# Kernel optimization log

Hardware: AMD Instinct MI355X
Metric: run time of the kernel (lower is better)

The kernel has to match this reference:

```python
import jax, jax.numpy as jnp
import numpy as np

N, E, HID, H_SA, H_MHA, L = 20000, 320000, 128, 4, 4, 32
MLP_HID = 4 * HID
EPS = 1e-6


def _ln(x, eps=EPS):
    mu = jnp.mean(x, axis=-1, keepdims=True)
    var = jnp.var(x, axis=-1, keepdims=True)
    return (x - mu) * jax.lax.rsqrt(var + eps)


def _modulate(x, shift, scale):
    return x * (1.0 + scale) + shift


def setup_inputs() -> dict:
    key = jax.random.key(0)
    ks = jax.random.split(key, 32)
    s = 0.02
    inp = {
        'x': jax.random.normal(ks[0], (N, HID), jnp.float32),
        'edge_index': jax.random.randint(ks[1], (2, E), 0, N, jnp.int64),
        't': jax.random.normal(ks[2], (N, HID), jnp.float32),
        'text_emb': jax.random.normal(ks[3], (N, L, HID), jnp.float32),
        # TransformerConv (per-head out_channels = HID, concat=False)
        'sa_q_w': jax.random.normal(ks[4], (HID, H_SA * HID), jnp.float32) * s,
        'sa_q_b': jnp.zeros((H_SA * HID,), jnp.float32),
        'sa_k_w': jax.random.normal(ks[5], (HID, H_SA * HID), jnp.float32) * s,
        'sa_k_b': jnp.zeros((H_SA * HID,), jnp.float32),
        'sa_v_w': jax.random.normal(ks[6], (HID, H_SA * HID), jnp.float32) * s,
        'sa_v_b': jnp.zeros((H_SA * HID,), jnp.float32),
        'sa_skip_w': jax.random.normal(ks[7], (HID, HID), jnp.float32) * s,
        'sa_skip_b': jnp.zeros((HID,), jnp.float32),
        # norm3 affine
        'n3_g': jnp.ones((HID,), jnp.float32),
        'n3_b': jnp.zeros((HID,), jnp.float32),
        # MultiheadAttention
        'mha_q_w': jax.random.normal(ks[8], (HID, HID), jnp.float32) * s,
        'mha_q_b': jnp.zeros((HID,), jnp.float32),
        'mha_k_w': jax.random.normal(ks[9], (HID, HID), jnp.float32) * s,
        'mha_k_b': jnp.zeros((HID,), jnp.float32),
        'mha_v_w': jax.random.normal(ks[10], (HID, HID), jnp.float32) * s,
        'mha_v_b': jnp.zeros((HID,), jnp.float32),
        'mha_o_w': jax.random.normal(ks[11], (HID, HID), jnp.float32) * s,
        'mha_o_b': jnp.zeros((HID,), jnp.float32),
        # MLP
        'fc1_w': jax.random.normal(ks[12], (HID, MLP_HID), jnp.float32) * s,
        'fc1_b': jnp.zeros((MLP_HID,), jnp.float32),
        'fc2_w': jax.random.normal(ks[13], (MLP_HID, HID), jnp.float32) * s,
        'fc2_b': jnp.zeros((HID,), jnp.float32),
        # adaLN modulation
        'ada_w': jax.random.normal(ks[14], (HID, 6 * HID), jnp.float32) * s,
        'ada_b': jnp.zeros((6 * HID,), jnp.float32),
    }
    return inp


def reference(x, edge_index, t, text_emb,
              sa_q_w, sa_q_b, sa_k_w, sa_k_b, sa_v_w, sa_v_b, sa_skip_w, sa_skip_b,
              n3_g, n3_b,
              mha_q_w, mha_q_b, mha_k_w, mha_k_b, mha_v_w, mha_v_b, mha_o_w, mha_o_b,
              fc1_w, fc1_b, fc2_w, fc2_b, ada_w, ada_b):
    n = x.shape[0]
    # adaLN: SiLU -> Linear -> chunk(6)
    mod = jax.nn.silu(t) @ ada_w + ada_b  # [N, 6*HID]
    shift_msa, scale_msa, gate_msa, shift_mlp, scale_mlp, gate_mlp = jnp.split(mod, 6, axis=1)

    # ---- graph self-attention (PyG TransformerConv, concat=False) ----
    xm = _modulate(_ln(x), shift_msa, scale_msa)  # [N, HID]
    q = (xm @ sa_q_w + sa_q_b).reshape(n, H_SA, HID)
    k = (xm @ sa_k_w + sa_k_b).reshape(n, H_SA, HID)
    v = (xm @ sa_v_w + sa_v_b).reshape(n, H_SA, HID)
    src, dst = edge_index[0], edge_index[1]  # messages flow src -> dst
    # per-edge attention logits [E, H]
    logits = jnp.einsum('ehd,ehd->eh', q[dst], k[src]) / jnp.sqrt(jnp.float32(HID))
    m = jax.ops.segment_max(logits, dst, num_segments=n)          # [N, H]
    ex = jnp.exp(logits - m[dst])                                  # [E, H]
    den = jax.ops.segment_sum(ex, dst, num_segments=n)            # [N, H]
    alpha = ex / den[dst]                                          # [E, H]
    agg = jax.ops.segment_sum(alpha[:, :, None] * v[src], dst, num_segments=n)  # [N, H, HID]
    sa_out = agg.mean(axis=1) + (xm @ sa_skip_w + sa_skip_b)       # concat=False -> head mean, + root skip
    x = x + gate_msa * sa_out

    # ---- cross attention: each node attends over its text memory ----
    qn = _ln(x) * n3_g + n3_b                                      # norm3 (affine)
    dh = HID // H_MHA
    qh = (qn @ mha_q_w + mha_q_b).reshape(n, H_MHA, dh)
    kh = (text_emb @ mha_k_w + mha_k_b).reshape(n, L, H_MHA, dh)
    vh = (text_emb @ mha_v_w + mha_v_b).reshape(n, L, H_MHA, dh)
    scores = jnp.einsum('nhd,nlhd->nhl', qh, kh) / jnp.sqrt(jnp.float32(dh))
    attn = jax.nn.softmax(scores, axis=-1)
    ctx = jnp.einsum('nhl,nlhd->nhd', attn, vh).reshape(n, HID)
    x = x + (ctx @ mha_o_w + mha_o_b)

    # ---- gated MLP ----
    xm2 = _modulate(_ln(x), shift_mlp, scale_mlp)
    h = jax.nn.gelu(xm2 @ fc1_w + fc1_b, approximate=True)
    x = x + gate_mlp * (h @ fc2_w + fc2_b)
    return x
```

## Files before the change

### kernel.cpp

```cpp
#include <hip/hip_runtime.h>
#include <hip/hip_bf16.h>
#include <math.h>

using ushort8 = __attribute__((ext_vector_type(8))) unsigned short;
using short8  = __attribute__((ext_vector_type(8))) short;
using f32x4   = __attribute__((ext_vector_type(4))) float;
using f32x2   = __attribute__((ext_vector_type(2))) float;

__device__ __forceinline__ float bf2f(unsigned short u) {
    union { unsigned int i; float f; } c; c.i = ((unsigned int)u) << 16; return c.f;
}
__device__ __forceinline__ unsigned short f2bf(float f) {
    __hip_bfloat16 h = __float2bfloat16(f);
    return *reinterpret_cast<unsigned short*>(&h);
}
__device__ __forceinline__ float silu_f(float x) { return x / (1.f + __expf(-x)); }
__device__ __forceinline__ float gelu_f(float x) {
    float x3 = x * x * x;
    return 0.5f * x * (1.f + tanhf(0.7978845608028654f * (x + 0.044715f * x3)));
}

constexpr int QKV_STRIDE_B = 2304;

template<int WM, int AIN, int PRE, int EPI, int OUTBF>
__global__ __launch_bounds__(256) void gemm_mfma(
    const void* __restrict__ Ain, const unsigned short* __restrict__ Wt,
    const float* __restrict__ bias, void* __restrict__ Cout,
    const float* __restrict__ res, const void* __restrict__ gatep,
    int Nrows, int K, int M)
{
    constexpr int BM = 32 * WM;
    __shared__ unsigned short As[BM][64];
    __shared__ unsigned short Bs[128][64];
    const int tid = threadIdx.x;
    const int row0 = blockIdx.x * BM;
    const int col0 = blockIdx.y * 128;
    const int lane = tid & 63;
    const int wid  = tid >> 6;
    const int wr = (wid >> 1) * 16 * WM;
    const int wc = (wid & 1) * 64;
    const int lr = lane & 15;
    const int lk = lane >> 4;

    f32x4 acc[WM][4];
#pragma unroll
    for (int i = 0; i < WM; i++)
#pragma unroll
        for (int j = 0; j < 4; j++) acc[i][j] = (f32x4)0.f;

    for (int k0 = 0; k0 < K; k0 += 64) {
#pragma unroll
        for (int i = 0; i < BM * 8 / 256; i++) {
            int f = tid + i * 256;
            int m = f >> 3, b = f & 7;
            int r = row0 + m;
            ushort8 h;
            if (r < Nrows) {
                if (AIN == 1) {
                    h = *(const ushort8*)((const unsigned short*)Ain + (size_t)r * K + k0 + b * 8);
                } else {
                    const float* ap = (const float*)Ain + (size_t)r * K + k0 + b * 8;
                    float4 p0 = *(const float4*)ap;
                    float4 p1 = *(const float4*)(ap + 4);
                    float v[8] = {p0.x, p0.y, p0.z, p0.w, p1.x, p1.y, p1.z, p1.w};
                    if (PRE == 1) {
#pragma unroll
                        for (int j = 0; j < 8; j++) v[j] = silu_f(v[j]);
                    }
#pragma unroll
                    for (int j = 0; j < 8; j++) h[j] = f2bf(v[j]);
                }
            } else {
#pragma unroll
                for (int j = 0; j < 8; j++) h[j] = 0;
            }
            *(ushort8*)&As[m][((b ^ (m & 7))) * 8] = h;
        }
#pragma unroll
        for (int i = 0; i < 4; i++) {
            int f = tid + i * 256;
            int n = f >> 3, b = f & 7;
            ushort8 w = *(const ushort8*)(Wt + (size_t)(col0 + n) * K + k0 + b * 8);
            *(ushort8*)&Bs[n][((b ^ (n & 7))) * 8] = w;
        }
        __syncthreads();

        short8 afr[WM][2], bfr[4][2];
#pragma unroll
        for (int fr = 0; fr < WM; fr++)
#pragma unroll
            for (int s = 0; s < 2; s++) {
                int m = wr + fr * 16 + lr;
                int blk = (s * 4 + lk) ^ (m & 7);
                afr[fr][s] = *(const short8*)&As[m][blk * 8];
            }
#pragma unroll
        for (int fc = 0; fc < 4; fc++)
#pragma unroll
            for (int s = 0; s < 2; s++) {
                int n = wc + fc * 16 + lr;
                int blk = (s * 4 + lk) ^ (n & 7);
                bfr[fc][s] = *(const short8*)&Bs[n][blk * 8];
            }
#pragma unroll
        for (int fr = 0; fr < WM; fr++)
#pragma unroll
            for (int fc = 0; fc < 4; fc++)
#pragma unroll
                for (int s = 0; s < 2; s++)
                    acc[fr][fc] = __builtin_amdgcn_mfma_f32_16x16x32_bf16(
                        afr[fr][s], bfr[fc][s], acc[fr][fc], 0, 0, 0);
        __syncthreads();
    }

#pragma unroll
    for (int fr = 0; fr < WM; fr++) {
#pragma unroll
        for (int fc = 0; fc < 4; fc++) {
#pragma unroll
            for (int r = 0; r < 4; r++) {
                int row = row0 + wr + fr * 16 + (lane >> 4) * 4 + r;
                if (row >= Nrows) continue;
                int col = col0 + wc + fc * 16 + (lane & 15);
                float val = acc[fr][fc][r] + bias[col];
                if (EPI == 4) {
                    unsigned char* rowp = (unsigned char*)Cout + (size_t)row * QKV_STRIDE_B;
                    if (col < 512) {
                        *(unsigned short*)(rowp + 2 * col) = f2bf(val);
                    } else if (col < 1536) {
                        int p = __builtin_amdgcn_cvt_pk_fp8_f32(val, 0.f, 0, false);
                        rowp[1024 + (col - 512)] = (unsigned char)(p & 0xff);
                    } else {
                        *(unsigned short*)(rowp + 2048 + 2 * (col - 1536)) = f2bf(val);
                    }
                } else {
                    size_t idx = (size_t)row * M + col;
                    if (EPI == 1) val = gelu_f(val);
                    else if (EPI == 2) val = res[idx] + val;
                    else if (EPI == 3) val = res[idx] +
                        bf2f(((const unsigned short*)gatep)[(size_t)row * 768 + col]) * val;
                    if (OUTBF) ((unsigned short*)Cout)[idx] = f2bf(val);
                    else       ((float*)Cout)[idx] = val;
                }
            }
        }
    }
}

__global__ __launch_bounds__(256) void prep_all(
    const float* __restrict__ qW, const float* __restrict__ qB,
    const float* __restrict__ kW, const float* __restrict__ kB,
    const float* __restrict__ vW, const float* __restrict__ vB,
    const float* __restrict__ sW, const float* __restrict__ sB,
    const float* __restrict__ f1W, const float* __restrict__ f2W,
    const float* __restrict__ adW,
    unsigned short* __restrict__ Wsa_t, float* __restrict__ bsa,
    unsigned short* __restrict__ fc1_t, unsigned short* __restrict__ fc2_t,
    unsigned short* __restrict__ ada_t,
    const float* __restrict__ Wq, const float* __restrict__ bq,
    const float* __restrict__ Wk, const float* __restrict__ Wv,
    const float* __restrict__ bv, const float* __restrict__ Wo,
    const float* __restrict__ bo,
    unsigned short* __restrict__ Mcat_t, float* __restrict__ biasM,
    unsigned short* __restrict__ Pcat_t, float* __restrict__ co)
{
    int g = blockIdx.x * 256 + threadIdx.x;
    if (g < 65536) {
        int m = g >> 7, kk = g & 127;
        Wsa_t[m * 128 + kk] = f2bf(qW[(size_t)kk * 512 + m]);
        if (kk == 0) bsa[m] = qB[m];
    } else if (g < 131072) {
        int l = g - 65536; int m = l >> 7, kk = l & 127;
        int p = 512 + ((m >> 2) << 3) + (m & 3);
        Wsa_t[p * 128 + kk] = f2bf(kW[(size_t)kk * 512 + m]);
        if (kk == 0) bsa[p] = kB[m];
    } else if (g < 196608) {
        int l = g - 131072; int m = l >> 7, kk = l & 127;
        int p = 516 + ((m >> 2) << 3) + (m & 3);
        Wsa_t[p * 128 + kk] = f2bf(vW[(size_t)kk * 512 + m]);
        if (kk == 0) bsa[p] = vB[m];
    } else if (g < 212992) {
        int l = g - 196608; int m = l >> 7, kk = l & 127;
        Wsa_t[(1536 + m) * 128 + kk] = f2bf(sW[(size_t)kk * 128 + m]);
        if (kk == 0) bsa[1536 + m] = sB[m];
    } else if (g < 278528) {
        int l = g - 212992; int m = l >> 7, kk = l & 127;
        fc1_t[m * 128 + kk] = f2bf(f1W[(size_t)kk * 512 + m]);
    } else if (g < 344064) {
        int l = g - 278528; int m = l >> 9, kk = l & 511;
        fc2_t[m * 512 + kk] = f2bf(f2W[(size_t)kk * 128 + m]);
    } else if (g < 442368) {
        int l = g - 344064; int m = l >> 7, kk = l & 127;
        ada_t[m * 128 + kk] = f2bf(adW[(size_t)kk * 768 + m]);
    } else {
        int g2 = g - 442368;
        {
            int i0 = g2 >> 9, col = g2 & 511, h = col >> 7, i = col & 127;
            float s = 0.f;
#pragma unroll 8
            for (int j = 0; j < 32; j++)
                s += Wq[i0 * 128 + h * 32 + j] * Wk[i * 128 + h * 32 + j];
            Mcat_t[col * 128 + i0] = f2bf(s);
        }
        {
            int rowp = g2 >> 7, j = g2 & 127, h = rowp >> 7, i = rowp & 127;
            float s = 0.f;
#pragma unroll 8
            for (int d = 0; d < 32; d++)
                s += Wv[i * 128 + h * 32 + d] * Wo[(h * 32 + d) * 128 + j];
            Pcat_t[j * 512 + rowp] = f2bf(s);
        }
        if (g2 < 512) {
            int h = g2 >> 7, i = g2 & 127;
            float s = 0.f;
            for (int j = 0; j < 32; j++)
                s += bq[h * 32 + j] * Wk[i * 128 + h * 32 + j];
            biasM[g2] = s;
        }
        if (g2 < 128) {
            float s = bo[g2];
            for (int m = 0; m < 128; m++) s += bv[m] * Wo[m * 128 + g2];
            co[g2] = s;
        }
    }
}

__global__ __launch_bounds__(256) void ln_mod_kernel(
    const float* __restrict__ x, const unsigned short* __restrict__ mod,
    int shift_off, int scale_off, unsigned short* __restrict__ outb, int N)
{
    int node = blockIdx.x * 4 + (threadIdx.x >> 6);
    if (node >= N) return;
    int lane = threadIdx.x & 63;
    f32x2 v = *(const f32x2*)(x + (size_t)node * 128 + lane * 2);
    float s = v[0] + v[1], ss = v[0] * v[0] + v[1] * v[1];
#pragma unroll
    for (int m = 1; m < 64; m <<= 1) { s += __shfl_xor(s, m); ss += __shfl_xor(ss, m); }
    float mu = s * (1.f / 128.f);
    float rs = rsqrtf(ss * (1.f / 128.f) - mu * mu + 1e-6f);
    const unsigned short* mp = mod + (size_t)node * 768;
    ushort2 sh = *(const ushort2*)(mp + shift_off + lane * 2);
    ushort2 sc = *(const ushort2*)(mp + scale_off + lane * 2);
    ushort2 o;
    o.x = f2bf((v[0] - mu) * rs * (1.f + bf2f(sc.x)) + bf2f(sh.x));
    o.y = f2bf((v[1] - mu) * rs * (1.f + bf2f(sc.y)) + bf2f(sh.y));
    *(ushort2*)(outb + (size_t)node * 128 + lane * 2) = o;
}

__global__ void count_edges(const int* __restrict__ dst, int* __restrict__ count, int E) {
    int e = blockIdx.x * blockDim.x + threadIdx.x;
    if (e < E) atomicAdd(&count[dst[e]], 1);
}

__global__ __launch_bounds__(1024) void scan_block(const int* __restrict__ cnt,
                                                   int* __restrict__ pre,
                                                   int* __restrict__ bsum, int n)
{
    __shared__ int tmp[1024];
    int gid = blockIdx.x * 1024 + threadIdx.x;
    int v = (gid < n) ? cnt[gid] : 0;
    tmp[threadIdx.x] = v;
    __syncthreads();
    for (int off = 1; off < 1024; off <<= 1) {
        int add = (threadIdx.x >= off) ? tmp[threadIdx.x - off] : 0;
        __syncthreads();
        tmp[threadIdx.x] += add;
        __syncthreads();
    }
    if (gid < n) pre[gid] = tmp[threadIdx.x];
    if (threadIdx.x == 1023) bsum[blockIdx.x] = tmp[1023];
}

__global__ void scan_tops(int* __restrict__ bsum, int nb) {
    if (threadIdx.x == 0 && blockIdx.x == 0) {
        int c = 0;
        for (int i = 0; i < nb; i++) { int v = bsum[i]; bsum[i] = c; c += v; }
    }
}

__global__ void scan_fix(const int* __restrict__ pre, const int* __restrict__ bsum,
                         const int* __restrict__ cnt,
                         int* __restrict__ base, int* __restrict__ cursor, int n)
{
    int gid = blockIdx.x * 256 + threadIdx.x;
    if (gid < n) {
        int inc = pre[gid] + bsum[gid >> 10];
        base[gid + 1] = inc;
        cursor[gid] = inc - cnt[gid];
    }
    if (gid == 0) base[0] = 0;
}

__global__ void scatter_edges(const int* __restrict__ src, const int* __restrict__ dst,
                              int* __restrict__ cursor, int* __restrict__ csr_src, int E) {
    int e = blockIdx.x * blockDim.x + threadIdx.x;
    if (e < E) {
        int pos = atomicAdd(&cursor[dst[e]], 1);
        csr_src[pos] = src[e];
    }
}

__global__ __launch_bounds__(128) void sa_node_kernel(
    const unsigned char* __restrict__ qkv,
    const int* __restrict__ base, const int* __restrict__ csr_src,
    const float* __restrict__ x, const unsigned short* __restrict__ mod,
    const float* __restrict__ n3g, const float* __restrict__ n3b,
    float* __restrict__ x1, unsigned short* __restrict__ qn)
{
    int node = blockIdx.x, t = threadIdx.x;
    const unsigned char* nrow = qkv + (size_t)node * QKV_STRIDE_B;
    ushort4 qu = *(const ushort4*)((const unsigned short*)nrow + t * 4);
    const float scl = 0.08838834764831845f;
    float q0 = bf2f(qu.x) * scl, q1 = bf2f(qu.y) * scl;
    float q2 = bf2f(qu.z) * scl, q3 = bf2f(qu.w) * scl;
    int beg = base[node], end = base[node + 1];
    float den = 0.f;
    float a0 = 0.f, a1 = 0.f, a2 = 0.f, a3 = 0.f;
    float b0 = 0.f, b1 = 0.f, b2 = 0.f, b3 = 0.f;
    uint2 c0 = make_uint2(0, 0), c1 = c0, c2 = c0, c3 = c0;
    if (beg < end)
        c0 = *(const uint2*)(qkv + (size_t)csr_src[beg] * QKV_STRIDE_B + 1024 + t * 8);
    if (beg + 1 < end)
        c1 = *(const uint2*)(qkv + (size_t)csr_src[beg + 1] * QKV_STRIDE_B + 1024 + t * 8);
    if (beg + 2 < end)
        c2 = *(const uint2*)(qkv + (size_t)csr_src[beg + 2] * QKV_STRIDE_B + 1024 + t * 8);
    if (beg + 3 < end)
        c3 = *(const uint2*)(qkv + (size_t)csr_src[beg + 3] * QKV_STRIDE_B + 1024 + t * 8);
    for (int e = beg; e < end; e += 4) {
        uint2 m0 = c0, m1 = c1, m2 = c2, m3 = c3;
        if (e + 4 < end)
            c0 = *(const uint2*)(qkv + (size_t)csr_src[e + 4] * QKV_STRIDE_B + 1024 + t * 8);
        if (e + 5 < end)
            c1 = *(const uint2*)(qkv + (size_t)csr_src[e + 5] * QKV_STRIDE_B + 1024 + t * 8);
        if (e + 6 < end)
            c2 = *(const uint2*)(qkv + (size_t)csr_src[e + 6] * QKV_STRIDE_B + 1024 + t * 8);
        if (e + 7 < end)
            c3 = *(const uint2*)(qkv + (size_t)csr_src[e + 7] * QKV_STRIDE_B + 1024 + t * 8);
        f32x2 k01, k23;
        k01 = __builtin_amdgcn_cvt_pk_f32_fp8(m0.x, false);
        k23 = __builtin_amdgcn_cvt_pk_f32_fp8(m0.x, true);
        float p0 = q0 * k01[0] + q1 * k01[1] + q2 * k23[0] + q3 * k23[1];
        k01 = __builtin_amdgcn_cvt_pk_f32_fp8(m1.x, false);
        k23 = __builtin_amdgcn_cvt_pk_f32_fp8(m1.x, true);
        float p1 = q0 * k01[0] + q1 * k01[1] + q2 * k23[0] + q3 * k23[1];
        k01 = __builtin_amdgcn_cvt_pk_f32_fp8(m2.x, false);
        k23 = __builtin_amdgcn_cvt_pk_f32_fp8(m2.x, true);
        float p2 = q0 * k01[0] + q1 * k01[1] + q2 * k23[0] + q3 * k23[1];
        k01 = __builtin_amdgcn_cvt_pk_f32_fp8(m3.x, false);
        k23 = __builtin_amdgcn_cvt_pk_f32_fp8(m3.x, true);
        float p3 = q0 * k01[0] + q1 * k01[1] + q2 * k23[0] + q3 * k23[1];
#pragma unroll
        for (int mm = 1; mm < 32; mm <<= 1) {
            p0 += __shfl_xor(p0, mm);
            p1 += __shfl_xor(p1, mm);
            p2 += __shfl_xor(p2, mm);
            p3 += __shfl_xor(p3, mm);
        }
        float pe0 = __expf(fminf(p0, 80.f));
        float pe1 = (e + 1 < end) ? __expf(fminf(p1, 80.f)) : 0.f;
        float pe2 = (e + 2 < end) ? __expf(fminf(p2, 80.f)) : 0.f;
        float pe3 = (e + 3 < end) ? __expf(fminf(p3, 80.f)) : 0.f;
        den += (pe0 + pe1) + (pe2 + pe3);
        f32x2 v01, v23;
        v01 = __builtin_amdgcn_cvt_pk_f32_fp8(m0.y, false);
        v23 = __builtin_amdgcn_cvt_pk_f32_fp8(m0.y, true);
        a0 += pe0 * v01[0]; a1 += pe0 * v01[1]; a2 += pe0 * v23[0]; a3 += pe0 * v23[1];
        v01 = __builtin_amdgcn_cvt_pk_f32_fp8(m1.y, false);
        v23 = __builtin_amdgcn_cvt_pk_f32_fp8(m1.y, true);
        b0 += pe1 * v01[0]; b1 += pe1 * v01[1]; b2 += pe1 * v23[0]; b3 += pe1 * v23[1];
        v01 = __builtin_amdgcn_cvt_pk_f32_fp8(m2.y, false);
        v23 = __builtin_amdgcn_cvt_pk_f32_fp8(m2.y, true);
        a0 += pe2 * v01[0]; a1 += pe2 * v01[1]; a2 += pe2 * v23[0]; a3 += pe2 * v23[1];
        v01 = __builtin_amdgcn_cvt_pk_f32_fp8(m3.y, false);
        v23 = __builtin_amdgcn_cvt_pk_f32_fp8(m3.y, true);
        b0 += pe3 * v01[0]; b1 += pe3 * v01[1]; b2 += pe3 * v23[0]; b3 += pe3 * v23[1];
    }
    a0 += b0; a1 += b1; a2 += b2; a3 += b3;
    float inv = (den > 0.f) ? 0.25f / den : 0.f;
    __shared__ float red[512];
    *(float4*)&red[t * 4] = make_float4(a0 * inv, a1 * inv, a2 * inv, a3 * inv);
    __syncthreads();
    float sa = red[t] + red[128 + t] + red[256 + t] + red[384 + t];
    float sab = bf2f(*(const unsigned short*)(nrow + 2048 + 2 * t));
    float g = bf2f(mod[(size_t)node * 768 + 256 + t]);
    size_t idx = (size_t)node * 128 + t;
    float xv = x[idx] + g * (sa + sab);
    x1[idx] = xv;
    float s = xv, ssq = xv * xv;
#pragma unroll
    for (int m = 1; m < 64; m <<= 1) { s += __shfl_xor(s, m); ssq += __shfl_xor(ssq, m); }
    __shared__ float l_s[2], l_ss[2];
    int w = t >> 6;
    if ((t & 63) == 0) { l_s[w] = s; l_ss[w] = ssq; }
    __syncthreads();
    float S = l_s[0] + l_s[1], SS = l_ss[0] + l_ss[1];
    float mu = S * (1.f / 128.f);
    float rs = rsqrtf(SS * (1.f / 128.f) - mu * mu + 1e-6f);
    qn[idx] = f2bf((xv - mu) * rs * n3g[t] + n3b[t]);
}

__global__ __launch_bounds__(128) void cross_mid_kernel(
    const float* __restrict__ te, const unsigned short* __restrict__ qw,
    unsigned short* __restrict__ u)
{
    int node = blockIdx.x, t = threadIdx.x;
    __shared__ float tes[32 * 132];
    __shared__ float qws[512];
    __shared__ float attnL[128];
#pragma unroll
    for (int i = 0; i < 8; i++) {
        int f = t + i * 128;
        int l = f >> 5, ii = (f & 31) * 4;
        float4 val = *(const float4*)(te + (size_t)node * 4096 + l * 128 + ii);
        *(float4*)&tes[l * 132 + ii] = val;
    }
    {
        ushort4 qv = *(const ushort4*)(qw + (size_t)node * 512 + t * 4);
        qws[t * 4 + 0] = bf2f(qv.x);
        qws[t * 4 + 1] = bf2f(qv.y);
        qws[t * 4 + 2] = bf2f(qv.z);
        qws[t * 4 + 3] = bf2f(qv.w);
    }
    __syncthreads();

    int h = t >> 5, l = t & 31;
    float sc = 0.f;
#pragma unroll
    for (int i = 0; i < 32; i++) {
        float4 tv = *(const float4*)&tes[l * 132 + i * 4];
        float4 qv4 = *(const float4*)&qws[h * 128 + i * 4];
        sc += tv.x * qv4.x + tv.y * qv4.y + tv.z * qv4.z + tv.w * qv4.w;
    }
    sc *= 0.17677669529663687f;
    float mx = sc;
#pragma unroll
    for (int mm = 1; mm < 32; mm <<= 1) mx = fmaxf(mx, __shfl_xor(mx, mm));
    float e = __expf(sc - mx);
    float ssum = e;
#pragma unroll
    for (int mm = 1; mm < 32; mm <<= 1) ssum += __shfl_xor(ssum, mm);
    attnL[t] = e / ssum;
    __syncthreads();

    int i0 = t & 31;
    float u0 = 0, u1 = 0, u2 = 0, u3 = 0;
#pragma unroll 4
    for (int ll = 0; ll < 32; ll++) {
        float a = attnL[h * 32 + ll];
        u0 += a * tes[ll * 132 + i0];
        u1 += a * tes[ll * 132 + i0 + 32];
        u2 += a * tes[ll * 132 + i0 + 64];
        u3 += a * tes[ll * 132 + i0 + 96];
    }
    size_t ub = (size_t)node * 512 + h * 128;
    u[ub + i0] = f2bf(u0);
    u[ub + i0 + 32] = f2bf(u1);
    u[ub + i0 + 64] = f2bf(u2);
    u[ub + i0 + 96] = f2bf(u3);
}

extern "C" void kernel_launch(void* const* d_in, const int* in_sizes, int n_in,
                              void* d_out, int out_size, void* d_ws, size_t ws_size,
                              hipStream_t stream)
{
    const int N = in_sizes[0] / 128;
    const int E = in_sizes[1] / 2;

    const float* x      = (const float*)d_in[0];
    const int*   ei     = (const int*)d_in[1];
    const float* t_in   = (const float*)d_in[2];
    const float* te     = (const float*)d_in[3];
    const float* sa_q_w = (const float*)d_in[4];
    const float* sa_q_b = (const float*)d_in[5];
    const float* sa_k_w = (const float*)d_in[6];
    const float* sa_k_b = (const float*)d_in[7];
    const float* sa_v_w = (const float*)d_in[8];
    const float* sa_v_b = (const float*)d_in[9];
    const float* sa_skip_w = (const float*)d_in[10];
    const float* sa_skip_b = (const float*)d_in[11];
    const float* n3_g   = (const float*)d_in[12];
    const float* n3_b   = (const float*)d_in[13];
    const float* mha_q_w = (const float*)d_in[14];
    const float* mha_q_b = (const float*)d_in[15];
    const float* mha_k_w = (const float*)d_in[16];
    const float* mha_v_w = (const float*)d_in[18];
    const float* mha_v_b = (const float*)d_in[19];
    const float* mha_o_w = (const float*)d_in[20];
    const float* mha_o_b = (const float*)d_in[21];
    const float* fc1_w  = (const float*)d_in[22];
    const float* fc1_b  = (const float*)d_in[23];
    const float* fc2_w  = (const float*)d_in[24];
    const float* fc2_b  = (const float*)d_in[25];
    const float* ada_w  = (const float*)d_in[26];
    const float* ada_b  = (const float*)d_in[27];
    float* out = (float*)d_out;

    float* ws = (float*)d_ws;
    size_t o = 0;
    unsigned short* modb = (unsigned short*)(ws + o); o += (size_t)N * 384;
    unsigned short* Bbuf = (unsigned short*)(ws + o); o += (size_t)N * 64;
    unsigned short* Qn   = (unsigned short*)(ws + o); o += (size_t)N * 64;
    unsigned short* Cbuf = (unsigned short*)(ws + o); o += (size_t)N * 256;
    unsigned short* Dbuf = (unsigned short*)(ws + o); o += (size_t)N * 256;
    unsigned short* Ebuf = (unsigned short*)(ws + o); o += (size_t)N * 256;
    float* Gbuf = ws + o; o += (size_t)N * 128;
    unsigned char* QKV = (unsigned char*)(ws + o); o += (size_t)N * (QKV_STRIDE_B / 4);
    unsigned short* Wsa_t  = (unsigned short*)(ws + o); o += 1664 * 128 / 2;
    unsigned short* Mcat_t = (unsigned short*)(ws + o); o += 512 * 128 / 2;
    unsigned short* Pcat_t = (unsigned short*)(ws + o); o += 128 * 512 / 2;
    unsigned short* fc1_t  = (unsigned short*)(ws + o); o += 512 * 128 / 2;
    unsigned short* fc2_t  = (unsigned short*)(ws + o); o += 128 * 512 / 2;
    unsigned short* ada_t  = (unsigned short*)(ws + o); o += 768 * 128 / 2;
    float* bsa   = ws + o; o += 1664;
    float* biasM = ws + o; o += 512;
    float* co    = ws + o; o += 128;
    int* count   = (int*)(ws + o); o += N;
    int* base    = (int*)(ws + o); o += N + 4;
    int* cursor  = (int*)(ws + o); o += N;
    int* pre     = (int*)(ws + o); o += N;
    int* bsum    = (int*)(ws + o); o += 32;
    int* csr_src = (int*)(ws + o); o += E;

    const int* src = ei;
    const int* dst = ei + E;
    const int rb128 = (N + 127) / 128;
    const int rb64  = (N + 63) / 64;
    const int nScan = (N + 1023) / 1024;

    prep_all<<<1984, 256, 0, stream>>>(sa_q_w, sa_q_b, sa_k_w, sa_k_b,
                                       sa_v_w, sa_v_b, sa_skip_w, sa_skip_b,
                                       fc1_w, fc2_w, ada_w,
                                       Wsa_t, bsa, fc1_t, fc2_t, ada_t,
                                       mha_q_w, mha_q_b, mha_k_w, mha_v_w,
                                       mha_v_b, mha_o_w, mha_o_b,
                                       Mcat_t, biasM, Pcat_t, co);

    hipMemsetAsync(count, 0, (size_t)N * sizeof(int), stream);
    count_edges<<<(E + 255) / 256, 256, 0, stream>>>(dst, count, E);
    scan_block<<<nScan, 1024, 0, stream>>>(count, pre, bsum, N);
    scan_tops<<<1, 64, 0, stream>>>(bsum, nScan);
    scan_fix<<<(N + 255) / 256, 256, 0, stream>>>(pre, bsum, count, base, cursor, N);
    scatter_edges<<<(E + 255) / 256, 256, 0, stream>>>(src, dst, cursor, csr_src, E);

    gemm_mfma<4, 0, 1, 0, 1><<<dim3(rb128, 6), 256, 0, stream>>>(
        t_in, ada_t, ada_b, modb, nullptr, nullptr, N, 128, 768);

    ln_mod_kernel<<<(N + 3) / 4, 256, 0, stream>>>(x, modb, 0, 128, Bbuf, N);

    gemm_mfma<4, 1, 0, 4, 1><<<dim3(rb128, 13), 256, 0, stream>>>(
        Bbuf, Wsa_t, bsa, QKV, nullptr, nullptr, N, 128, 1664);

    sa_node_kernel<<<N, 128, 0, stream>>>(QKV, base, csr_src, x, modb,
                                          n3_g, n3_b, Gbuf, Qn);

    gemm_mfma<4, 1, 0, 0, 1><<<dim3(rb128, 4), 256, 0, stream>>>(
        Qn, Mcat_t, biasM, Cbuf, nullptr, nullptr, N, 128, 512);
    cross_mid_kernel<<<N, 128, 0, stream>>>(te, Cbuf, Dbuf);
    gemm_mfma<2, 1, 0, 2, 0><<<dim3(rb64, 1), 256, 0, stream>>>(
        Dbuf, Pcat_t, co, Gbuf, Gbuf, nullptr, N, 512, 128);

    ln_mod_kernel<<<(N + 3) / 4, 256, 0, stream>>>(Gbuf, modb, 384, 512, Bbuf, N);
    gemm_mfma<4, 1, 0, 1, 1><<<dim3(rb128, 4), 256, 0, stream>>>(
        Bbuf, fc1_t, fc1_b, Ebuf, nullptr, nullptr, N, 128, 512);
    gemm_mfma<2, 1, 0, 3, 0><<<dim3(rb64, 1), 256, 0, stream>>>(
        Ebuf, fc2_t, fc2_b, out, Gbuf, modb + 640, N, 512, 128);
}
```

Before: 378.6 us.

## Regroup fp8 K/V layout for 16-byte gathers and use one wave per node

The prep kernel now interleaves K and V for each head in 8-element fp8 groups, so one 16-byte load brings 8 K and 8 V values for a lane. sa_node_kernel uses a single 64-thread wave per node, with 16 lanes per head, 2-edge prefetching and shuffle-only reductions instead of shared-memory reductions and barriers. The separate scan_tops launch is folded into scan_fix, which makes every block recompute the block offsets serially. These changes aim to cut gather instructions, block overhead and one kernel launch, at the cost of less edge-level prefetch depth and more registers per thread.

```diff
diff --git a/kernel.cpp b/kernel.cpp
--- a/kernel.cpp
+++ b/kernel.cpp
@@ -171,12 +171,14 @@
         if (kk == 0) bsa[m] = qB[m];
     } else if (g < 131072) {
         int l = g - 65536; int m = l >> 7, kk = l & 127;
-        int p = 512 + ((m >> 2) << 3) + (m & 3);
+        int h = m >> 7, dl = m & 127;
+        int p = 512 + h * 256 + ((dl >> 3) << 4) + (dl & 7);
         Wsa_t[p * 128 + kk] = f2bf(kW[(size_t)kk * 512 + m]);
         if (kk == 0) bsa[p] = kB[m];
     } else if (g < 196608) {
         int l = g - 131072; int m = l >> 7, kk = l & 127;
-        int p = 516 + ((m >> 2) << 3) + (m & 3);
+        int h = m >> 7, dl = m & 127;
+        int p = 512 + h * 256 + ((dl >> 3) << 4) + 8 + (dl & 7);
         Wsa_t[p * 128 + kk] = f2bf(vW[(size_t)kk * 512 + m]);
         if (kk == 0) bsa[p] = vB[m];
     } else if (g < 212992) {
@@ -271,20 +273,20 @@
     if (threadIdx.x == 1023) bsum[blockIdx.x] = tmp[1023];
 }
 
-__global__ void scan_tops(int* __restrict__ bsum, int nb) {
-    if (threadIdx.x == 0 && blockIdx.x == 0) {
-        int c = 0;
-        for (int i = 0; i < nb; i++) { int v = bsum[i]; bsum[i] = c; c += v; }
-    }
-}
-
 __global__ void scan_fix(const int* __restrict__ pre, const int* __restrict__ bsum,
                          const int* __restrict__ cnt,
-                         int* __restrict__ base, int* __restrict__ cursor, int n)
-{
+                         int* __restrict__ base, int* __restrict__ cursor,
+                         int n, int nb)
+{
+    __shared__ int boff[32];
+    if (threadIdx.x == 0) {
+        int c = 0;
+        for (int i = 0; i < nb; i++) { boff[i] = c; c += bsum[i]; }
+    }
+    __syncthreads();
     int gid = blockIdx.x * 256 + threadIdx.x;
     if (gid < n) {
-        int inc = pre[gid] + bsum[gid >> 10];
+        int inc = pre[gid] + boff[gid >> 10];
         base[gid + 1] = inc;
         cursor[gid] = inc - cnt[gid];
     }
@@ -300,103 +302,106 @@
     }
 }
 
-__global__ __launch_bounds__(128) void sa_node_kernel(
+__global__ __launch_bounds__(64) void sa_node_kernel(
     const unsigned char* __restrict__ qkv,
     const int* __restrict__ base, const int* __restrict__ csr_src,
     const float* __restrict__ x, const unsigned short* __restrict__ mod,
     const float* __restrict__ n3g, const float* __restrict__ n3b,
     float* __restrict__ x1, unsigned short* __restrict__ qn)
 {
-    int node = blockIdx.x, t = threadIdx.x;
+    int node = blockIdx.x, l = threadIdx.x;
     const unsigned char* nrow = qkv + (size_t)node * QKV_STRIDE_B;
-    ushort4 qu = *(const ushort4*)((const unsigned short*)nrow + t * 4);
+    ushort8 qu = *(const ushort8*)(nrow + l * 16);
     const float scl = 0.08838834764831845f;
-    float q0 = bf2f(qu.x) * scl, q1 = bf2f(qu.y) * scl;
-    float q2 = bf2f(qu.z) * scl, q3 = bf2f(qu.w) * scl;
+    float q[8];
+#pragma unroll
+    for (int j = 0; j < 8; j++) q[j] = bf2f(qu[j]) * scl;
     int beg = base[node], end = base[node + 1];
     float den = 0.f;
-    float a0 = 0.f, a1 = 0.f, a2 = 0.f, a3 = 0.f;
-    float b0 = 0.f, b1 = 0.f, b2 = 0.f, b3 = 0.f;
-    uint2 c0 = make_uint2(0, 0), c1 = c0, c2 = c0, c3 = c0;
+    float a[8];
+#pragma unroll
+    for (int j = 0; j < 8; j++) a[j] = 0.f;
+    uint4 c0 = make_uint4(0, 0, 0, 0), c1 = c0;
     if (beg < end)
-        c0 = *(const uint2*)(qkv + (size_t)csr_src[beg] * QKV_STRIDE_B + 1024 + t * 8);
+        c0 = *(const uint4*)(qkv + (size_t)csr_src[beg] * QKV_STRIDE_B + 1024 + l * 16);
     if (beg + 1 < end)
-        c1 = *(const uint2*)(qkv + (size_t)csr_src[beg + 1] * QKV_STRIDE_B + 1024 + t * 8);
-    if (beg + 2 < end)
-        c2 = *(const uint2*)(qkv + (size_t)csr_src[beg + 2] * QKV_STRIDE_B + 1024 + t * 8);
-    if (beg + 3 < end)
-        c3 = *(const uint2*)(qkv + (size_t)csr_src[beg + 3] * QKV_STRIDE_B + 1024 + t * 8);
-    for (int e = beg; e < end; e += 4) {
-        uint2 m0 = c0, m1 = c1, m2 = c2, m3 = c3;
-        if (e + 4 < end)
-            c0 = *(const uint2*)(qkv + (size_t)csr_src[e + 4] * QKV_STRIDE_B + 1024 + t * 8);
-        if (e + 5 < end)
-            c1 = *(const uint2*)(qkv + (size_t)csr_src[e + 5] * QKV_STRIDE_B + 1024 + t * 8);
-        if (e + 6 < end)
-            c2 = *(const uint2*)(qkv + (size_t)csr_src[e + 6] * QKV_STRIDE_B + 1024 + t * 8);
-        if (e + 7 < end)
-            c3 = *(const uint2*)(qkv + (size_t)csr_src[e + 7] * QKV_STRIDE_B + 1024 + t * 8);
-        f32x2 k01, k23;
-        k01 = __builtin_amdgcn_cvt_pk_f32_fp8(m0.x, false);
-        k23 = __builtin_amdgcn_cvt_pk_f32_fp8(m0.x, true);
-        float p0 = q0 * k01[0] + q1 * k01[1] + q2 * k23[0] + q3 * k23[1];
-        k01 = __builtin_amdgcn_cvt_pk_f32_fp8(m1.x, false);
-        k23 = __builtin_amdgcn_cvt_pk_f32_fp8(m1.x, true);
-        float p1 = q0 * k01[0] + q1 * k01[1] + q2 * k23[0] + q3 * k23[1];
-        k01 = __builtin_amdgcn_cvt_pk_f32_fp8(m2.x, false);
-        k23 = __builtin_amdgcn_cvt_pk_f32_fp8(m2.x, true);
-        float p2 = q0 * k01[0] + q1 * k01[1] + q2 * k23[0] + q3 * k23[1];
-        k01 = __builtin_amdgcn_cvt_pk_f32_fp8(m3.x, false);
-        k23 = __builtin_amdgcn_cvt_pk_f32_fp8(m3.x, true);
-        float p3 = q0 * k01[0] + q1 * k01[1] + q2 * k23[0] + q3 * k23[1];
-#pragma unroll
-        for (int mm = 1; mm < 32; mm <<= 1) {
+        c1 = *(const uint4*)(qkv + (size_t)csr_src[beg + 1] * QKV_STRIDE_B + 1024 + l * 16);
+    for (int e = beg; e < end; e += 2) {
+        uint4 m0 = c0, m1 = c1;
+        if (e + 2 < end)
+            c0 = *(const uint4*)(qkv + (size_t)csr_src[e + 2] * QKV_STRIDE_B + 1024 + l * 16);
+        if (e + 3 < end)
+            c1 = *(const uint4*)(qkv + (size_t)csr_src[e + 3] * QKV_STRIDE_B + 1024 + l * 16);
+        f32x2 kA, kB, kC, kD;
+        kA = __builtin_amdgcn_cvt_pk_f32_fp8(m0.x, false);
+        kB = __builtin_amdgcn_cvt_pk_f32_fp8(m0.x, true);
+        kC = __builtin_amdgcn_cvt_pk_f32_fp8(m0.y, false);
+        kD = __builtin_amdgcn_cvt_pk_f32_fp8(m0.y, true);
+        float p0 = q[0]*kA[0] + q[1]*kA[1] + q[2]*kB[0] + q[3]*kB[1]
+                 + q[4]*kC[0] + q[5]*kC[1] + q[6]*kD[0] + q[7]*kD[1];
+        kA = __builtin_amdgcn_cvt_pk_f32_fp8(m1.x, false);
+        kB = __builtin_amdgcn_cvt_pk_f32_fp8(m1.x, true);
+        kC = __builtin_amdgcn_cvt_pk_f32_fp8(m1.y, false);
+        kD = __builtin_amdgcn_cvt_pk_f32_fp8(m1.y, true);
+        float p1 = q[0]*kA[0] + q[1]*kA[1] + q[2]*kB[0] + q[3]*kB[1]
+                 + q[4]*kC[0] + q[5]*kC[1] + q[6]*kD[0] + q[7]*kD[1];
+#pragma unroll
+        for (int mm = 1; mm < 16; mm <<= 1) {
             p0 += __shfl_xor(p0, mm);
             p1 += __shfl_xor(p1, mm);
-            p2 += __shfl_xor(p2, mm);
-            p3 += __shfl_xor(p3, mm);
         }
         float pe0 = __expf(fminf(p0, 80.f));
         float pe1 = (e + 1 < end) ? __expf(fminf(p1, 80.f)) : 0.f;
-        float pe2 = (e + 2 < end) ? __expf(fminf(p2, 80.f)) : 0.f;
-        float pe3 = (e + 3 < end) ? __expf(fminf(p3, 80.f)) : 0.f;
-        den += (pe0 + pe1) + (pe2 + pe3);
-        f32x2 v01, v23;
-        v01 = __builtin_amdgcn_cvt_pk_f32_fp8(m0.y, false);
-        v23 = __builtin_amdgcn_cvt_pk_f32_fp8(m0.y, true);
-        a0 += pe0 * v01[0]; a1 += pe0 * v01[1]; a2 += pe0 * v23[0]; a3 += pe0 * v23[1];
-        v01 = __builtin_amdgcn_cvt_pk_f32_fp8(m1.y, false);
-        v23 = __builtin_amdgcn_cvt_pk_f32_fp8(m1.y, true);
-        b0 += pe1 * v01[0]; b1 += pe1 * v01[1]; b2 += pe1 * v23[0]; b3 += pe1 * v23[1];
-        v01 = __builtin_amdgcn_cvt_pk_f32_fp8(m2.y, false);
-        v23 = __builtin_amdgcn_cvt_pk_f32_fp8(m2.y, true);
-        a0 += pe2 * v01[0]; a1 += pe2 * v01[1]; a2 += pe2 * v23[0]; a3 += pe2 * v23[1];
-        v01 = __builtin_amdgcn_cvt_pk_f32_fp8(m3.y, false);
-        v23 = __builtin_amdgcn_cvt_pk_f32_fp8(m3.y, true);
-        b0 += pe3 * v01[0]; b1 += pe3 * v01[1]; b2 += pe3 * v23[0]; b3 += pe3 * v23[1];
-    }
-    a0 += b0; a1 += b1; a2 += b2; a3 += b3;
+        den += pe0 + pe1;
+        f32x2 vA, vB, vC, vD, wA, wB, wC, wD;
+        vA = __builtin_amdgcn_cvt_pk_f32_fp8(m0.z, false);
+        vB = __builtin_amdgcn_cvt_pk_f32_fp8(m0.z, true);
+        vC = __builtin_amdgcn_cvt_pk_f32_fp8(m0.w, false);
+        vD = __builtin_amdgcn_cvt_pk_f32_fp8(m0.w, true);
+        wA = __builtin_amdgcn_cvt_pk_f32_fp8(m1.z, false);
+        wB = __builtin_amdgcn_cvt_pk_f32_fp8(m1.z, true);
+        wC = __builtin_amdgcn_cvt_pk_f32_fp8(m1.w, false);
+        wD = __builtin_amdgcn_cvt_pk_f32_fp8(m1.w, true);
+        a[0] += pe0 * vA[0] + pe1 * wA[0];
+        a[1] += pe0 * vA[1] + pe1 * wA[1];
+        a[2] += pe0 * vB[0] + pe1 * wB[0];
+        a[3] += pe0 * vB[1] + pe1 * wB[1];
+        a[4] += pe0 * vC[0] + pe1 * wC[0];
+        a[5] += pe0 * vC[1] + pe1 * wC[1];
+        a[6] += pe0 * vD[0] + pe1 * wD[0];
+        a[7] += pe0 * vD[1] + pe1 * wD[1];
+    }
     float inv = (den > 0.f) ? 0.25f / den : 0.f;
-    __shared__ float red[512];
-    *(float4*)&red[t * 4] = make_float4(a0 * inv, a1 * inv, a2 * inv, a3 * inv);
+    __shared__ float sa_sh[128];
+#pragma unroll
+    for (int j = 0; j < 8; j++) {
+        float s = a[j] * inv;
+        s += __shfl_xor(s, 16);
+        s += __shfl_xor(s, 32);
+        a[j] = s;
+    }
+    if (l < 16) {
+#pragma unroll
+        for (int j = 0; j < 8; j++) sa_sh[l * 8 + j] = a[j];
+    }
     __syncthreads();
-    float sa = red[t] + red[128 + t] + red[256 + t] + red[384 + t];
-    float sab = bf2f(*(const unsigned short*)(nrow + 2048 + 2 * t));
-    float g = bf2f(mod[(size_t)node * 768 + 256 + t]);
-    size_t idx = (size_t)node * 128 + t;
-    float xv = x[idx] + g * (sa + sab);
-    x1[idx] = xv;
-    float s = xv, ssq = xv * xv;
+    f32x2 sa2 = *(const f32x2*)&sa_sh[l * 2];
+    ushort2 sk = *(const ushort2*)(nrow + 2048 + l * 4);
+    ushort2 gt = *(const ushort2*)(mod + (size_t)node * 768 + 256 + l * 2);
+    f32x2 xv2 = *(const f32x2*)(x + (size_t)node * 128 + l * 2);
+    float xv0 = xv2[0] + bf2f(gt.x) * (sa2[0] + bf2f(sk.x));
+    float xv1 = xv2[1] + bf2f(gt.y) * (sa2[1] + bf2f(sk.y));
+    f32x2 xo; xo[0] = xv0; xo[1] = xv1;
+    *(f32x2*)(x1 + (size_t)node * 128 + l * 2) = xo;
+    float s = xv0 + xv1, ssq = xv0 * xv0 + xv1 * xv1;
 #pragma unroll
     for (int m = 1; m < 64; m <<= 1) { s += __shfl_xor(s, m); ssq += __shfl_xor(ssq, m); }
-    __shared__ float l_s[2], l_ss[2];
-    int w = t >> 6;
-    if ((t & 63) == 0) { l_s[w] = s; l_ss[w] = ssq; }
-    __syncthreads();
-    float S = l_s[0] + l_s[1], SS = l_ss[0] + l_ss[1];
-    float mu = S * (1.f / 128.f);
-    float rs = rsqrtf(SS * (1.f / 128.f) - mu * mu + 1e-6f);
-    qn[idx] = f2bf((xv - mu) * rs * n3g[t] + n3b[t]);
+    float mu = s * (1.f / 128.f);
+    float rs = rsqrtf(ssq * (1.f / 128.f) - mu * mu + 1e-6f);
+    ushort2 qo;
+    qo.x = f2bf((xv0 - mu) * rs * n3g[l * 2] + n3b[l * 2]);
+    qo.y = f2bf((xv1 - mu) * rs * n3g[l * 2 + 1] + n3b[l * 2 + 1]);
+    *(ushort2*)(qn + (size_t)node * 128 + l * 2) = qo;
 }
 
 __global__ __launch_bounds__(128) void cross_mid_kernel(
@@ -538,8 +543,7 @@
     hipMemsetAsync(count, 0, (size_t)N * sizeof(int), stream);
     count_edges<<<(E + 255) / 256, 256, 0, stream>>>(dst, count, E);
     scan_block<<<nScan, 1024, 0, stream>>>(count, pre, bsum, N);
-    scan_tops<<<1, 64, 0, stream>>>(bsum, nScan);
-    scan_fix<<<(N + 255) / 256, 256, 0, stream>>>(pre, bsum, count, base, cursor, N);
+    scan_fix<<<(N + 255) / 256, 256, 0, stream>>>(pre, bsum, count, base, cursor, N, nScan);
     scatter_edges<<<(E + 255) / 256, 256, 0, stream>>>(src, dst, cursor, csr_src, E);
 
     gemm_mfma<4, 0, 1, 0, 1><<<dim3(rb128, 6), 256, 0, stream>>>(
@@ -550,8 +554,8 @@
     gemm_mfma<4, 1, 0, 4, 1><<<dim3(rb128, 13), 256, 0, stream>>>(
         Bbuf, Wsa_t, bsa, QKV, nullptr, nullptr, N, 128, 1664);
 
-    sa_node_kernel<<<N, 128, 0, stream>>>(QKV, base, csr_src, x, modb,
-                                          n3_g, n3_b, Gbuf, Qn);
+    sa_node_kernel<<<N, 64, 0, stream>>>(QKV, base, csr_src, x, modb,
+                                         n3_g, n3_b, Gbuf, Qn);
 
     gemm_mfma<4, 1, 0, 0, 1><<<dim3(rb128, 4), 256, 0, stream>>>(
         Qn, Mcat_t, biasM, Cbuf, nullptr, nullptr, N, 128, 512);
```

New measurement: 375.9 us. Within noise of the previous version (-0.7%).
